# Kernel optimization log

Measured on AMD Instinct MI355X. Metric: run time of the kernel, lower is better.

Reference implementation:

```python
import jax, jax.numpy as jnp
import numpy as np

E, H, I, R, T, TOPK = 8, 1024, 2816, 8, 4096, 2
SCALING = 2.0  # lora_alpha / r = 16 / 8


def setup_inputs() -> dict:
    key = jax.random.key(0)
    ks = jax.random.split(key, 12)
    inp = {
        "hidden_states": jax.random.normal(ks[0], (T, H), dtype=jnp.float32),
        "routing_weights": jax.random.uniform(ks[1], (T, TOPK), dtype=jnp.float32),
        "selected_experts": jax.random.randint(ks[2], (T, TOPK), 0, E),
        # frozen base expert weights, (G, K, N) layout
        "gate_proj": jax.random.normal(ks[3], (E, H, I), dtype=jnp.float32) * 0.02,
        "up_proj": jax.random.normal(ks[4], (E, H, I), dtype=jnp.float32) * 0.02,
        "down_proj": jax.random.normal(ks[5], (E, I, H), dtype=jnp.float32) * 0.02,
        # LoRA adapters, A: [E, in, r], B: [E, r, out]  (B random, not zero, so delta is exercised)
        "gate_A": jax.random.normal(ks[6], (E, H, R), dtype=jnp.float32) * 0.02,
        "gate_B": jax.random.normal(ks[7], (E, R, I), dtype=jnp.float32) * 0.02,
        "up_A": jax.random.normal(ks[8], (E, H, R), dtype=jnp.float32) * 0.02,
        "up_B": jax.random.normal(ks[9], (E, R, I), dtype=jnp.float32) * 0.02,
        "down_A": jax.random.normal(ks[10], (E, I, R), dtype=jnp.float32) * 0.02,
        "down_B": jax.random.normal(ks[11], (E, R, H), dtype=jnp.float32) * 0.02,
    }
    return inp


def _moe_lora_forward(x, routing_weights, selected_experts,
                      gate_proj, up_proj, down_proj,
                      gate_A, gate_B, up_A, up_B, down_A, down_B):
    # combine weights per (token, expert): [T, E]
    combine = jnp.sum(
        jax.nn.one_hot(selected_experts, E, dtype=x.dtype) * routing_weights[..., None],
        axis=1,
    )
    out = jnp.zeros_like(x)
    for e in range(E):  # static small loop over experts
        g = x @ gate_proj[e] + SCALING * ((x @ gate_A[e]) @ gate_B[e])
        u = x @ up_proj[e] + SCALING * ((x @ up_A[e]) @ up_B[e])
        h = jax.nn.silu(g) * u  # [T, I]
        y = h @ down_proj[e] + SCALING * ((h @ down_A[e]) @ down_B[e])  # [T, H]
        out = out + combine[:, e:e + 1] * y
    return out


def reference(hidden_states, routing_weights, selected_experts,
              gate_proj, up_proj, down_proj,
              gate_A, gate_B, up_A, up_B, down_A, down_B):
    return _moe_lora_forward(hidden_states, routing_weights, selected_experts,
                             gate_proj, up_proj, down_proj,
                             gate_A, gate_B, up_A, up_B, down_A, down_B)
```

## Files before the change

### kernel.cpp

```cpp
#include <hip/hip_runtime.h>
#include <stdint.h>

#define T_TOK 4096
#define NE 8
#define HH 1024
#define II 2816
#define HE 1056
#define IEW 2944
#define HT 23
#define RRK 8
#define NPAIR (T_TOK*2)
#define ROWCAP 10240
#define MT_MAX 40
#define SCAL 2.0f

typedef short v8s __attribute__((ext_vector_type(8)));
typedef float v4f __attribute__((ext_vector_type(4)));

__device__ __forceinline__ unsigned short f2bf(float f){
  union { float f; unsigned u; } c; c.f = f;
  unsigned u = c.u;
  u += 0x7FFFu + ((u >> 16) & 1u);
  return (unsigned short)(u >> 16);
}
__device__ __forceinline__ float bf2f(unsigned short h){
  union { unsigned u; float f; } c; c.u = ((unsigned)h) << 16;
  return c.f;
}
__device__ __forceinline__ void gload16(const void* g, void* l){
  __builtin_amdgcn_global_load_lds(
      (const __attribute__((address_space(1))) unsigned int*)g,
      (__attribute__((address_space(3))) unsigned int*)l, 16, 0, 0);
}
__device__ __forceinline__ void fence_(){ asm volatile("" ::: "memory"); }

__global__ void route_count(const int* __restrict__ sel, int* __restrict__ counts,
                            int* __restrict__ bases, int* __restrict__ tile_e,
                            int* __restrict__ tile_r0){
  __shared__ int c[NE];
  int tid = threadIdx.x;
  if (tid < NE) c[tid] = 0;
  __syncthreads();
  for (int p = tid; p < NPAIR; p += 256) atomicAdd(&c[sel[p]], 1);
  __syncthreads();
  if (tid == 0){
    int b = 0;
    for (int e = 0; e < NE; e++){ counts[e] = c[e]; bases[e] = b; b += ((c[e] + 255) >> 8) << 8; }
    bases[NE] = b;
    int t = 0;
    for (int e = 0; e < NE; e++){
      int nt = (c[e] + 255) >> 8;
      for (int i = 0; i < nt; i++){ tile_e[t] = e; tile_r0[t] = bases[e] + i * 256; t++; }
    }
    for (; t < MT_MAX; t++){ tile_e[t] = -1; tile_r0[t] = 0; }
  }
}

__global__ void route_fill(const int* __restrict__ sel, const float* __restrict__ rw,
                           const int* __restrict__ bases,
                           int* __restrict__ row_token, int* __restrict__ row_expert,
                           float* __restrict__ row_w, int* __restrict__ pair2row){
  int e = blockIdx.x;
  int lane = threadIdx.x;
  if (e == NE){
    for (int idx = bases[NE] + lane; idx < ROWCAP; idx += 64){
      row_token[idx] = -1; row_expert[idx] = 0; row_w[idx] = 0.f;
    }
    return;
  }
  int base = bases[e];
  int cnt = 0;
  for (int chunk = 0; chunk < NPAIR; chunk += 64){
    int p = chunk + lane;
    bool m = (sel[p] == e);
    unsigned long long mask = __ballot(m);
    if (m){
      int pos = __popcll(mask & ((1ull << lane) - 1ull));
      int dst = base + cnt + pos;
      row_token[dst] = p >> 1;
      row_expert[dst] = e;
      row_w[dst] = rw[p];
      pair2row[p] = dst;
    }
    cnt += __popcll(mask);
  }
  int nb = bases[e + 1];
  for (int idx = base + cnt + lane; idx < nb; idx += 64){
    row_token[idx] = -1; row_expert[idx] = e; row_w[idx] = 0.f;
  }
}

__device__ __forceinline__ void transpose_body32(const float* __restrict__ W,
                                                 unsigned short* __restrict__ Wt,
                                                 int K, int N, int KE, int e, int bid){
  int tilesK = K >> 5;
  int kt = (bid % tilesK) * 32;
  int nt = (bid / tilesK) * 64;
  __shared__ float tile[32][65];
  int tid = threadIdx.x;
  int r = tid >> 3;
  int c0 = (tid & 7) * 8;
  const float* src = W + (size_t)e * K * N + (size_t)(kt + r) * N + nt + c0;
  float4 v0 = *(const float4*)(src);
  float4 v1 = *(const float4*)(src + 4);
  *(float4*)&tile[r][c0]     = v0;
  *(float4*)&tile[r][c0 + 4] = v1;
  __syncthreads();
  int n = tid >> 2;
  int kc = (tid & 3) * 8;
  union { unsigned short us[8]; uint4 q; } pk;
  #pragma unroll
  for (int j = 0; j < 8; j++) pk.us[j] = f2bf(tile[kc + j][n]);
  unsigned short* dst = Wt + (size_t)e * N * KE + (size_t)(nt + n) * KE + kt + kc;
  *(uint4*)(dst) = pk.q;
}

__global__ void wprep(const float* __restrict__ gate_proj, const float* __restrict__ up_proj,
                      const float* __restrict__ down_proj,
                      const float* __restrict__ gB, const float* __restrict__ uB,
                      const float* __restrict__ dB,
                      unsigned short* __restrict__ Wtg, unsigned short* __restrict__ Wtu,
                      unsigned short* __restrict__ Wtd,
                      const float* __restrict__ x, const float* __restrict__ gA,
                      const float* __restrict__ uA, const int* __restrict__ row_token,
                      const int* __restrict__ row_expert, unsigned short* __restrict__ Xg){
  int b = blockIdx.x;
  if (b < 11264){
    transpose_body32(gate_proj, Wtg, HH, II, HE, b / 1408, b % 1408);
  } else if (b < 22528){
    b -= 11264;
    transpose_body32(up_proj, Wtu, HH, II, HE, b / 1408, b % 1408);
  } else if (b < 33792){
    b -= 22528;
    transpose_body32(down_proj, Wtd, II, HH, IEW, b / 1408, b % 1408);
  } else if (b < 33880){
    int idx = (b - 33792) * 256 + threadIdx.x;
    if (idx >= NE * II) return;
    int e = idx / II, n = idx % II;
    unsigned short* g = Wtg + ((size_t)e * II + n) * HE + HH;
    unsigned short* u = Wtu + ((size_t)e * II + n) * HE + HH;
    #pragma unroll
    for (int j = 0; j < 8; j++){
      g[j] = f2bf(gB[((size_t)e * RRK + j) * II + n]);
      u[j] = 0;
      g[8 + j] = 0;
      u[8 + j] = f2bf(uB[((size_t)e * RRK + j) * II + n]);
    }
    #pragma unroll
    for (int j = 16; j < 32; j++){ g[j] = 0; u[j] = 0; }
  } else if (b < 33912){
    int idx = (b - 33880) * 256 + threadIdx.x;
    if (idx >= NE * HH) return;
    int e = idx / HH, n = idx % HH;
    unsigned short* d = Wtd + ((size_t)e * HH + n) * IEW + II;
    #pragma unroll
    for (int j = 0; j < 8; j++) d[j] = f2bf(dB[((size_t)e * RRK + j) * HH + n]);
    for (int j = 8; j < 128; j++) d[j] = 0;
  } else {
    int p = b - 33912;
    int tid = threadIdx.x;
    int tok = row_token[p]; int e = row_expert[p];
    int k0 = tid * 4;
    float4 xv = make_float4(0.f, 0.f, 0.f, 0.f);
    if (tok >= 0) xv = *(const float4*)(x + (size_t)tok * HH + k0);
    uint2 o;
    o.x = (unsigned)f2bf(xv.x) | ((unsigned)f2bf(xv.y) << 16);
    o.y = (unsigned)f2bf(xv.z) | ((unsigned)f2bf(xv.w) << 16);
    *(uint2*)(Xg + (size_t)p * HE + k0) = o;

    float ag[8], au[8];
    #pragma unroll
    for (int r = 0; r < 8; r++){ ag[r] = 0.f; au[r] = 0.f; }
    if (tok >= 0){
      const float* pg = gA + ((size_t)e * HH + k0) * RRK;
      const float* pu = uA + ((size_t)e * HH + k0) * RRK;
      float xs[4] = {xv.x, xv.y, xv.z, xv.w};
      #pragma unroll
      for (int j = 0; j < 4; j++){
        #pragma unroll
        for (int r = 0; r < 8; r++){
          ag[r] += xs[j] * pg[j * RRK + r];
          au[r] += xs[j] * pu[j * RRK + r];
        }
      }
    }
    __shared__ float redg[8][4], redu[8][4];
    int lane = tid & 63, wv = tid >> 6;
    #pragma unroll
    for (int r = 0; r < 8; r++){
      float v1 = ag[r], v2 = au[r];
      for (int off = 32; off > 0; off >>= 1){ v1 += __shfl_down(v1, off); v2 += __shfl_down(v2, off); }
      if (lane == 0){ redg[r][wv] = v1; redu[r][wv] = v2; }
    }
    __syncthreads();
    if (tid < 8)
      Xg[(size_t)p * HE + HH + tid] = f2bf(SCAL * (redg[tid][0] + redg[tid][1] + redg[tid][2] + redg[tid][3]));
    else if (tid < 16){
      int r = tid - 8;
      Xg[(size_t)p * HE + HH + 8 + r] = f2bf(SCAL * (redu[r][0] + redu[r][1] + redu[r][2] + redu[r][3]));
    } else if (tid < 32){
      Xg[(size_t)p * HE + HH + tid] = 0;
    }
  }
}

__global__ void ha_kernel(const unsigned short* __restrict__ hbuf, const float* __restrict__ dA,
                          const int* __restrict__ row_expert, unsigned short* __restrict__ hout){
  int p = blockIdx.x; int tid = threadIdx.x;
  int e = row_expert[p];
  float a[8];
  #pragma unroll
  for (int r = 0; r < 8; r++) a[r] = 0.f;
  for (int i = 0; i < 11; i++){
    int k = i * 256 + tid;
    float hv = bf2f(hbuf[(size_t)(k >> 7) * (ROWCAP * 128) + (size_t)p * 128 + (k & 127)]);
    const float* pd = dA + ((size_t)e * II + k) * RRK;
    #pragma unroll
    for (int r = 0; r < 8; r++) a[r] += hv * pd[r];
  }
  __shared__ float red[8][4];
  int lane = tid & 63, wv = tid >> 6;
  #pragma unroll
  for (int r = 0; r < 8; r++){
    float v = a[r];
    for (int off = 32; off > 0; off >>= 1) v += __shfl_down(v, off);
    if (lane == 0) red[r][wv] = v;
  }
  __syncthreads();
  unsigned short* ext = hout + (size_t)22 * (ROWCAP * 128) + (size_t)p * 128;
  if (tid < 8)
    ext[tid] = f2bf(SCAL * (red[tid][0] + red[tid][1] + red[tid][2] + red[tid][3]));
  else if (tid < 128)
    ext[tid] = 0;
}

__launch_bounds__(512, 2)
__global__ void gemm1_kernel(const unsigned short* __restrict__ Xg,
                             const unsigned short* __restrict__ Wtg,
                             const unsigned short* __restrict__ Wtu,
                             const int* __restrict__ tile_e,
                             const int* __restrict__ tile_r0,
                             unsigned short* __restrict__ hbuf){
  int hw = blockIdx.x;
  int lg = (hw & 7) * 110 + (hw >> 3);
  int mt = lg / 22;
  int n0 = (lg % 22) * 128;

  int e = tile_e[mt];
  if (e < 0) return;
  int row0 = tile_r0[mt];

  __shared__ unsigned short lds[2][4 * 4096];
  int tid = threadIdx.x;
  int lane = tid & 63;
  int w = tid >> 6;
  int wm = w >> 1;
  int wn = w & 1;
  int g = lane >> 4, r16 = lane & 15;

  const unsigned short* srcA = Xg + (size_t)row0 * HE;
  const unsigned short* srcG = Wtg + ((size_t)e * II + n0) * HE;
  const unsigned short* srcU = Wtu + ((size_t)e * II + n0) * HE;

  v4f accg[4][4], accu[4][4];
  #pragma unroll
  for (int i = 0; i < 4; i++)
    #pragma unroll
    for (int j = 0; j < 4; j++){
      accg[i][j] = (v4f){0.f, 0.f, 0.f, 0.f};
      accu[i][j] = (v4f){0.f, 0.f, 0.f, 0.f};
    }

  int uA0 = tid, uA1 = tid + 512;
  int rA0 = uA0 >> 2, rA1 = uA1 >> 2;
  size_t gA0 = (size_t)rA0 * HE + ((uA0 & 3) ^ ((rA0 >> 1) & 3)) * 8;
  size_t gA1 = (size_t)rA1 * HE + ((uA1 & 3) ^ ((rA1 >> 1) & 3)) * 8;
  int lA0 = (uA0 & ~63) * 8, lA1 = (uA1 & ~63) * 8;
  int rB = tid >> 2;
  size_t gB = (size_t)rB * HE + ((tid & 3) ^ ((rB >> 1) & 3)) * 8;
  int lB = (tid & ~63) * 8;

  const int NT = HE / 32;

  {
    unsigned short* buf = lds[0];
    gload16(srcA + gA0, buf + lA0);
    gload16(srcA + gA1, buf + lA1);
    gload16(srcG + gB, buf + 8192 + lB);
    gload16(srcU + gB, buf + 12288 + lB);
  }

  for (int t = 0; t < NT; t++){
    if (t + 1 < NT){
      unsigned short* nbuf = lds[(t + 1) & 1];
      int ks = (t + 1) * 32;
      gload16(srcA + gA0 + ks, nbuf + lA0);
      gload16(srcA + gA1 + ks, nbuf + lA1);
      gload16(srcG + gB + ks, nbuf + 8192 + lB);
      gload16(srcU + gB + ks, nbuf + 12288 + lB);
      asm volatile("s_waitcnt vmcnt(4)" ::: "memory");
    } else {
      asm volatile("s_waitcnt vmcnt(0)" ::: "memory");
    }
    __builtin_amdgcn_s_barrier();
    fence_();
    const unsigned short* buf = lds[t & 1];
    v8s a[4], bg[4], bu[4];
    #pragma unroll
    for (int f = 0; f < 4; f++){
      int rowA = wm * 64 + f * 16 + r16;
      int ca = g ^ ((rowA >> 1) & 3);
      a[f] = *(const v8s*)(buf + rowA * 32 + ca * 8);
      int rowB = wn * 64 + f * 16 + r16;
      int cb = g ^ ((rowB >> 1) & 3);
      bg[f] = *(const v8s*)(buf + 8192 + rowB * 32 + cb * 8);
      bu[f] = *(const v8s*)(buf + 12288 + rowB * 32 + cb * 8);
    }
    #pragma unroll
    for (int fm = 0; fm < 4; fm++)
      #pragma unroll
      for (int fn = 0; fn < 4; fn++){
        accg[fm][fn] = __builtin_amdgcn_mfma_f32_16x16x32_bf16(a[fm], bg[fn], accg[fm][fn], 0, 0, 0);
        accu[fm][fn] = __builtin_amdgcn_mfma_f32_16x16x32_bf16(a[fm], bu[fn], accu[fm][fn], 0, 0, 0);
      }
    fence_();
    __builtin_amdgcn_s_barrier();
    fence_();
  }

  unsigned short* sh = (unsigned short*)lds;
  #pragma unroll
  for (int fm = 0; fm < 4; fm++)
    #pragma unroll
    for (int fn = 0; fn < 4; fn++)
      #pragma unroll
      for (int r = 0; r < 4; r++){
        int lrow = wm * 64 + fm * 16 + g * 4 + r;
        int lcol = wn * 64 + fn * 16 + r16;
        float gg = accg[fm][fn][r];
        float uu = accu[fm][fn][r];
        float hh = (gg / (1.f + __expf(-gg))) * uu;
        int ch = (lcol >> 3) ^ (lrow & 7);
        sh[lrow * 128 + ch * 8 + (lcol & 7)] = f2bf(hh);
      }
  __syncthreads();
  unsigned short* dst = hbuf + ((size_t)(n0 >> 7) * ROWCAP + row0) * 128;
  #pragma unroll
  for (int pass = 0; pass < 8; pass++){
    int idx2 = pass * 512 + tid;
    int row = idx2 >> 4;
    int ch = idx2 & 15;
    int chs = ch ^ (row & 7);
    v8s val = *(const v8s*)(sh + row * 128 + chs * 8);
    *(v8s*)(dst + row * 128 + ch * 8) = val;
  }
}

__launch_bounds__(512, 2)
__global__ void gemm2_kernel(const unsigned short* __restrict__ hbuf,
                             const unsigned short* __restrict__ Wtd,
                             const int* __restrict__ tile_e,
                             const int* __restrict__ tile_r0,
                             const float* __restrict__ row_w,
                             unsigned short* __restrict__ Y4){
  int hw = blockIdx.x;
  int lg = (hw & 7) * 80 + (hw >> 3);
  int mt = lg / 16;
  int rem = lg % 16;
  int n0 = (rem >> 2) * 256;
  int q = rem & 3;

  int e = tile_e[mt];
  if (e < 0) return;
  int row0 = tile_r0[mt];

  __shared__ unsigned short lds[2][2 * 8192];
  int tid = threadIdx.x;
  int lane = tid & 63;
  int w = tid >> 6;
  int wm = w >> 1;
  int wn = w & 1;
  int g = lane >> 4, r16 = lane & 15;

  const unsigned short* srcA = hbuf + (size_t)row0 * 128;
  const unsigned short* srcB = Wtd + ((size_t)e * HH + n0) * IEW;

  v4f acc[4][8];
  #pragma unroll
  for (int i = 0; i < 4; i++)
    #pragma unroll
    for (int j = 0; j < 8; j++) acc[i][j] = (v4f){0.f, 0.f, 0.f, 0.f};

  int u0 = tid, u1 = tid + 512;
  int r0_ = u0 >> 2, r1_ = u1 >> 2;
  int c0_ = (u0 & 3) ^ ((r0_ >> 1) & 3), c1_ = (u1 & 3) ^ ((r1_ >> 1) & 3);
  size_t aoff0 = (size_t)r0_ * 128 + c0_ * 8;
  size_t aoff1 = (size_t)r1_ * 128 + c1_ * 8;
  size_t boff0 = (size_t)r0_ * IEW + c0_ * 8;
  size_t boff1 = (size_t)r1_ * IEW + c1_ * 8;
  int l0 = (u0 & ~63) * 8, l1 = (u1 & ~63) * 8;

  const int NQ = (IEW / 32) / 4;
  int tbeg = q * NQ;
  int tend = tbeg + NQ;

  auto stage = [&](int t, unsigned short* buf){
    int ks = t * 32;
    size_t abase = (size_t)(ks >> 7) * (ROWCAP * 128) + (ks & 127);
    gload16(srcA + abase + aoff0, buf + l0);
    gload16(srcA + abase + aoff1, buf + l1);
    gload16(srcB + (size_t)ks + boff0, buf + 8192 + l0);
    gload16(srcB + (size_t)ks + boff1, buf + 8192 + l1);
  };

  stage(tbeg, lds[tbeg & 1]);

  for (int t = tbeg; t < tend; t++){
    if (t + 1 < tend){
      stage(t + 1, lds[(t + 1) & 1]);
      asm volatile("s_waitcnt vmcnt(4)" ::: "memory");
    } else {
      asm volatile("s_waitcnt vmcnt(0)" ::: "memory");
    }
    __builtin_amdgcn_s_barrier();
    fence_();
    const unsigned short* buf = lds[t & 1];
    v8s a[4], b[8];
    #pragma unroll
    for (int f = 0; f < 4; f++){
      int rowA = wm * 64 + f * 16 + r16;
      int ca = g ^ ((rowA >> 1) & 3);
      a[f] = *(const v8s*)(buf + rowA * 32 + ca * 8);
    }
    #pragma unroll
    for (int fn = 0; fn < 8; fn++){
      int rowB = wn * 128 + fn * 16 + r16;
      int cb = g ^ ((rowB >> 1) & 3);
      b[fn] = *(const v8s*)(buf + 8192 + rowB * 32 + cb * 8);
    }
    #pragma unroll
    for (int fm = 0; fm < 4; fm++)
      #pragma unroll
      for (int fn = 0; fn < 8; fn++)
        acc[fm][fn] = __builtin_amdgcn_mfma_f32_16x16x32_bf16(a[fm], b[fn], acc[fm][fn], 0, 0, 0);
    fence_();
    __builtin_amdgcn_s_barrier();
    fence_();
  }

  unsigned short* Yh = Y4 + (size_t)q * ROWCAP * HH;
  #pragma unroll
  for (int fm = 0; fm < 4; fm++){
    #pragma unroll
    for (int r = 0; r < 4; r++){
      int lrow = wm * 64 + fm * 16 + g * 4 + r;
      int grow = row0 + lrow;
      float wgt = row_w[grow];
      #pragma unroll
      for (int fn = 0; fn < 8; fn++){
        int lcol = wn * 128 + fn * 16 + r16;
        Yh[(size_t)grow * HH + n0 + lcol] = f2bf(wgt * acc[fm][fn][r]);
      }
    }
  }
}

__global__ void combine_kernel(const unsigned short* __restrict__ Y4,
                               const int* __restrict__ pair2row,
                               float* __restrict__ out){
  int t = blockIdx.x;
  int c = threadIdx.x * 4;
  int r0 = pair2row[2 * t];
  int r1 = pair2row[2 * t + 1];
  float s0 = 0.f, s1 = 0.f, s2 = 0.f, s3 = 0.f;
  #pragma unroll
  for (int q = 0; q < 4; q++){
    const unsigned short* Yh = Y4 + (size_t)q * ROWCAP * HH;
    uint2 a = *(const uint2*)(Yh + (size_t)r0 * HH + c);
    uint2 b = *(const uint2*)(Yh + (size_t)r1 * HH + c);
    s0 += bf2f((unsigned short)(a.x & 0xffff)) + bf2f((unsigned short)(b.x & 0xffff));
    s1 += bf2f((unsigned short)(a.x >> 16))    + bf2f((unsigned short)(b.x >> 16));
    s2 += bf2f((unsigned short)(a.y & 0xffff)) + bf2f((unsigned short)(b.y & 0xffff));
    s3 += bf2f((unsigned short)(a.y >> 16))    + bf2f((unsigned short)(b.y >> 16));
  }
  *(float4*)(out + (size_t)t * HH + c) = make_float4(s0, s1, s2, s3);
}

extern "C" void kernel_launch(void* const* d_in, const int* in_sizes, int n_in,
                              void* d_out, int out_size, void* d_ws, size_t ws_size,
                              hipStream_t stream){
  const float* x         = (const float*)d_in[0];
  const float* rw        = (const float*)d_in[1];
  const int*   sel       = (const int*)d_in[2];
  const float* gate_proj = (const float*)d_in[3];
  const float* up_proj   = (const float*)d_in[4];
  const float* down_proj = (const float*)d_in[5];
  const float* gate_A    = (const float*)d_in[6];
  const float* gate_B    = (const float*)d_in[7];
  const float* up_A      = (const float*)d_in[8];
  const float* up_B      = (const float*)d_in[9];
  const float* down_A    = (const float*)d_in[10];
  const float* down_B    = (const float*)d_in[11];
  float* out = (float*)d_out;
  char* ws = (char*)d_ws;

  constexpr size_t OFF_COUNTS = 0;
  constexpr size_t OFF_BASES  = 256;
  constexpr size_t OFF_TILE_E = 512;
  constexpr size_t OFF_TILE_R0 = 1024;
  constexpr size_t OFF_ROWTOK = 2048;
  constexpr size_t OFF_ROWEXP = OFF_ROWTOK + (size_t)ROWCAP * 4;
  constexpr size_t OFF_ROWW   = OFF_ROWEXP + (size_t)ROWCAP * 4;
  constexpr size_t OFF_P2R    = OFF_ROWW + (size_t)ROWCAP * 4;
  constexpr size_t OFF_XG     = OFF_P2R + (size_t)NPAIR * 4;
  constexpr size_t OFF_H      = OFF_XG + (size_t)ROWCAP * HE * 2;
  constexpr size_t OFF_WTG    = OFF_H + (size_t)HT * ROWCAP * 128 * 2;
  constexpr size_t OFF_WTU    = OFF_WTG + (size_t)NE * II * HE * 2;
  constexpr size_t OFF_WTD    = OFF_WTU + (size_t)NE * II * HE * 2;
  constexpr size_t OFF_Y      = OFF_WTG;

  int* counts    = (int*)(ws + OFF_COUNTS);
  int* bases     = (int*)(ws + OFF_BASES);
  int* tile_e    = (int*)(ws + OFF_TILE_E);
  int* tile_r0   = (int*)(ws + OFF_TILE_R0);
  int* row_token = (int*)(ws + OFF_ROWTOK);
  int* row_expert= (int*)(ws + OFF_ROWEXP);
  float* row_w   = (float*)(ws + OFF_ROWW);
  int* pair2row  = (int*)(ws + OFF_P2R);
  unsigned short* Xg   = (unsigned short*)(ws + OFF_XG);
  unsigned short* hbuf = (unsigned short*)(ws + OFF_H);
  unsigned short* Wtg  = (unsigned short*)(ws + OFF_WTG);
  unsigned short* Wtu  = (unsigned short*)(ws + OFF_WTU);
  unsigned short* Wtd  = (unsigned short*)(ws + OFF_WTD);
  unsigned short* Y4 = (unsigned short*)(ws + OFF_Y);

  route_count<<<1, 256, 0, stream>>>(sel, counts, bases, tile_e, tile_r0);
  route_fill<<<NE + 1, 64, 0, stream>>>(sel, rw, bases, row_token, row_expert, row_w, pair2row);
  wprep<<<33912 + ROWCAP, 256, 0, stream>>>(gate_proj, up_proj, down_proj, gate_B, up_B, down_B,
                                            Wtg, Wtu, Wtd, x, gate_A, up_A,
                                            row_token, row_expert, Xg);
  gemm1_kernel<<<MT_MAX * (II / 128), 512, 0, stream>>>(Xg, Wtg, Wtu, tile_e, tile_r0, hbuf);
  ha_kernel<<<ROWCAP, 256, 0, stream>>>(hbuf, down_A, row_expert, hbuf);
  gemm2_kernel<<<MT_MAX * (HH / 256) * 4, 512, 0, stream>>>(hbuf, Wtd, tile_e, tile_r0, row_w, Y4);
  combine_kernel<<<T_TOK, 256, 0, stream>>>(Y4, pair2row, out);
}
```

Before: 521.5 us.

## Overlap down_proj weight transpose with gemm1 by merging into one launch

Moves the down_proj transpose/bf16 conversion and down_B packing out of the weight-prep kernel and into extra blocks appended to the gemm1 grid. The intent is to let memory-bound transpose work overlap with compute-bound gemm1 tiles, and to shorten the prep kernel that sits on the critical path. Transpose blocks now use 512 threads, each doing two 256-thread sub-tiles, and draw on the 64KB shared allocation. The risk is that the heavy shared-memory footprint and co-scheduling contend with gemm1 occupancy. Another risk is that the transpose blocks, launched after the gemm blocks, run mostly serially at the tail.

```diff
diff --git a/kernel.cpp b/kernel.cpp
--- a/kernel.cpp
+++ b/kernel.cpp
@@ -90,24 +90,23 @@
   }
 }
 
-__device__ __forceinline__ void transpose_body32(const float* __restrict__ W,
-                                                 unsigned short* __restrict__ Wt,
-                                                 int K, int N, int KE, int e, int bid){
+__device__ __forceinline__ void transpose_sub32(const float* __restrict__ W,
+                                                unsigned short* __restrict__ Wt,
+                                                int K, int N, int KE, int e, int bid,
+                                                float (*tile)[65], int t256){
   int tilesK = K >> 5;
   int kt = (bid % tilesK) * 32;
   int nt = (bid / tilesK) * 64;
-  __shared__ float tile[32][65];
-  int tid = threadIdx.x;
-  int r = tid >> 3;
-  int c0 = (tid & 7) * 8;
+  int r = t256 >> 3;
+  int c0 = (t256 & 7) * 8;
   const float* src = W + (size_t)e * K * N + (size_t)(kt + r) * N + nt + c0;
   float4 v0 = *(const float4*)(src);
   float4 v1 = *(const float4*)(src + 4);
   *(float4*)&tile[r][c0]     = v0;
   *(float4*)&tile[r][c0 + 4] = v1;
   __syncthreads();
-  int n = tid >> 2;
-  int kc = (tid & 3) * 8;
+  int n = t256 >> 2;
+  int kc = (t256 & 3) * 8;
   union { unsigned short us[8]; uint4 q; } pk;
   #pragma unroll
   for (int j = 0; j < 8; j++) pk.us[j] = f2bf(tile[kc + j][n]);
@@ -115,26 +114,22 @@
   *(uint4*)(dst) = pk.q;
 }
 
-__global__ void wprep(const float* __restrict__ gate_proj, const float* __restrict__ up_proj,
-                      const float* __restrict__ down_proj,
-                      const float* __restrict__ gB, const float* __restrict__ uB,
-                      const float* __restrict__ dB,
-                      unsigned short* __restrict__ Wtg, unsigned short* __restrict__ Wtu,
-                      unsigned short* __restrict__ Wtd,
-                      const float* __restrict__ x, const float* __restrict__ gA,
-                      const float* __restrict__ uA, const int* __restrict__ row_token,
-                      const int* __restrict__ row_expert, unsigned short* __restrict__ Xg){
+__global__ void wprep1(const float* __restrict__ gate_proj, const float* __restrict__ up_proj,
+                       const float* __restrict__ gB, const float* __restrict__ uB,
+                       unsigned short* __restrict__ Wtg, unsigned short* __restrict__ Wtu,
+                       const float* __restrict__ x, const float* __restrict__ gA,
+                       const float* __restrict__ uA, const int* __restrict__ row_token,
+                       const int* __restrict__ row_expert, unsigned short* __restrict__ Xg){
+  __shared__ float tile[32][65];
   int b = blockIdx.x;
+  int tid = threadIdx.x;
   if (b < 11264){
-    transpose_body32(gate_proj, Wtg, HH, II, HE, b / 1408, b % 1408);
+    transpose_sub32(gate_proj, Wtg, HH, II, HE, b / 1408, b % 1408, tile, tid);
   } else if (b < 22528){
     b -= 11264;
-    transpose_body32(up_proj, Wtu, HH, II, HE, b / 1408, b % 1408);
-  } else if (b < 33792){
-    b -= 22528;
-    transpose_body32(down_proj, Wtd, II, HH, IEW, b / 1408, b % 1408);
-  } else if (b < 33880){
-    int idx = (b - 33792) * 256 + threadIdx.x;
+    transpose_sub32(up_proj, Wtu, HH, II, HE, b / 1408, b % 1408, tile, tid);
+  } else if (b < 22616){
+    int idx = (b - 22528) * 256 + tid;
     if (idx >= NE * II) return;
     int e = idx / II, n = idx % II;
     unsigned short* g = Wtg + ((size_t)e * II + n) * HE + HH;
@@ -148,17 +143,8 @@
     }
     #pragma unroll
     for (int j = 16; j < 32; j++){ g[j] = 0; u[j] = 0; }
-  } else if (b < 33912){
-    int idx = (b - 33880) * 256 + threadIdx.x;
-    if (idx >= NE * HH) return;
-    int e = idx / HH, n = idx % HH;
-    unsigned short* d = Wtd + ((size_t)e * HH + n) * IEW + II;
-    #pragma unroll
-    for (int j = 0; j < 8; j++) d[j] = f2bf(dB[((size_t)e * RRK + j) * HH + n]);
-    for (int j = 8; j < 128; j++) d[j] = 0;
   } else {
-    int p = b - 33912;
-    int tid = threadIdx.x;
+    int p = b - 22616;
     int tok = row_token[p]; int e = row_expert[p];
     int k0 = tid * 4;
     float4 xv = make_float4(0.f, 0.f, 0.f, 0.f);
@@ -235,13 +221,39 @@
 }
 
 __launch_bounds__(512, 2)
-__global__ void gemm1_kernel(const unsigned short* __restrict__ Xg,
-                             const unsigned short* __restrict__ Wtg,
-                             const unsigned short* __restrict__ Wtu,
-                             const int* __restrict__ tile_e,
-                             const int* __restrict__ tile_r0,
-                             unsigned short* __restrict__ hbuf){
-  int hw = blockIdx.x;
+__global__ void g1dp_kernel(const unsigned short* __restrict__ Xg,
+                            const unsigned short* __restrict__ Wtg,
+                            const unsigned short* __restrict__ Wtu,
+                            const int* __restrict__ tile_e,
+                            const int* __restrict__ tile_r0,
+                            unsigned short* __restrict__ hbuf,
+                            const float* __restrict__ down_proj,
+                            const float* __restrict__ dB,
+                            unsigned short* __restrict__ Wtd){
+  __shared__ char smem[65536];
+  int b = blockIdx.x;
+  int tid = threadIdx.x;
+
+  if (b >= 880){
+    if (b < 880 + 5632){
+      float (*tiles)[32][65] = (float (*)[32][65])smem;
+      int bid2 = (b - 880) * 2 + (tid >> 8);
+      int e = bid2 / 1408, inner = bid2 % 1408;
+      transpose_sub32(down_proj, Wtd, II, HH, IEW, e, inner, tiles[tid >> 8], tid & 255);
+    } else {
+      int idx = (b - 880 - 5632) * 512 + tid;
+      if (idx >= NE * HH) return;
+      int e = idx / HH, n = idx % HH;
+      unsigned short* d = Wtd + ((size_t)e * HH + n) * IEW + II;
+      #pragma unroll
+      for (int j = 0; j < 8; j++) d[j] = f2bf(dB[((size_t)e * RRK + j) * HH + n]);
+      for (int j = 8; j < 128; j++) d[j] = 0;
+    }
+    return;
+  }
+
+  unsigned short (*lds)[4 * 4096] = (unsigned short (*)[4 * 4096])smem;
+  int hw = b;
   int lg = (hw & 7) * 110 + (hw >> 3);
   int mt = lg / 22;
   int n0 = (lg % 22) * 128;
@@ -250,8 +262,6 @@
   if (e < 0) return;
   int row0 = tile_r0[mt];
 
-  __shared__ unsigned short lds[2][4 * 4096];
-  int tid = threadIdx.x;
   int lane = tid & 63;
   int w = tid >> 6;
   int wm = w >> 1;
@@ -328,7 +338,7 @@
     fence_();
   }
 
-  unsigned short* sh = (unsigned short*)lds;
+  unsigned short* sh = (unsigned short*)smem;
   #pragma unroll
   for (int fm = 0; fm < 4; fm++)
     #pragma unroll
@@ -536,10 +546,10 @@
 
   route_count<<<1, 256, 0, stream>>>(sel, counts, bases, tile_e, tile_r0);
   route_fill<<<NE + 1, 64, 0, stream>>>(sel, rw, bases, row_token, row_expert, row_w, pair2row);
-  wprep<<<33912 + ROWCAP, 256, 0, stream>>>(gate_proj, up_proj, down_proj, gate_B, up_B, down_B,
-                                            Wtg, Wtu, Wtd, x, gate_A, up_A,
-                                            row_token, row_expert, Xg);
-  gemm1_kernel<<<MT_MAX * (II / 128), 512, 0, stream>>>(Xg, Wtg, Wtu, tile_e, tile_r0, hbuf);
+  wprep1<<<22616 + ROWCAP, 256, 0, stream>>>(gate_proj, up_proj, gate_B, up_B, Wtg, Wtu,
+                                             x, gate_A, up_A, row_token, row_expert, Xg);
+  g1dp_kernel<<<880 + 5632 + 16, 512, 0, stream>>>(Xg, Wtg, Wtu, tile_e, tile_r0, hbuf,
+                                                   down_proj, down_B, Wtd);
   ha_kernel<<<ROWCAP, 256, 0, stream>>>(hbuf, down_A, row_expert, hbuf);
   gemm2_kernel<<<MT_MAX * (HH / 256) * 4, 512, 0, stream>>>(hbuf, Wtd, tile_e, tile_r0, row_w, Y4);
   combine_kernel<<<T_TOK, 256, 0, stream>>>(Y4, pair2row, out);
```

After: 532.1 us. 1.02x slower.
